# Kernel tuning notes

Hardware: AMD Instinct MI355X
Metric: run time of the kernel (lower is better)

## Reference

```python
import jax, jax.numpy as jnp
import numpy as np

N_NODES = 100000
N_EDGES = 3200000
N_GRAPHS = 1024
F_IN = 16
H = 64
N_CLASSES = 2
EPS = 1e-5


def _seg_sum(x, ids, n):
    return jax.ops.segment_sum(x, ids, num_segments=n, indices_are_sorted=True)


def graph_norm(x, batch, weight, bias, mean_scale, n_graphs):
    # PyG GraphNorm: per-graph mean (scaled by learnable mean_scale) and variance
    cnt = jnp.maximum(_seg_sum(jnp.ones((x.shape[0], 1), x.dtype), batch, n_graphs), 1.0)
    mean = _seg_sum(x, batch, n_graphs) / cnt                      # [G, F]
    out = x - mean[batch] * mean_scale                             # [N, F]
    var = _seg_sum(out * out, batch, n_graphs) / cnt               # [G, F]
    out = out / jnp.sqrt(var + EPS)[batch]
    return weight * out + bias


def graph_conv(x, src, dst, w_rel, b_rel, w_root):
    # PyG GraphConv (aggr='add'): lin_rel(sum_{j->i} x_j) + lin_root(x_i)
    agg = jax.ops.segment_sum(x[src], dst, num_segments=x.shape[0])  # [N, F_in]
    return agg @ w_rel.T + b_rel + x @ w_root.T


def setup_inputs():
    key = jax.random.key(0)
    ks = jax.random.split(key, 32)

    def lin(k, o, i):
        return jax.random.normal(k, (o, i), jnp.float32) * (1.0 / np.sqrt(i))

    inp = {}
    inp['x'] = jax.random.normal(ks[0], (N_NODES, F_IN), jnp.float32)
    inp['edge_index'] = jax.random.randint(ks[1], (2, N_EDGES), 0, N_NODES, jnp.int32)
    inp['batch'] = jnp.sort(jax.random.randint(ks[2], (N_NODES,), 0, N_GRAPHS, jnp.int32))
    # GraphNorm params (weight, bias, mean_scale), initialized as in PyG
    for name, f in (('gn0', F_IN), ('gn1', H), ('gn2', H)):
        inp[name + '_w'] = jnp.ones((f,), jnp.float32)
        inp[name + '_b'] = jnp.zeros((f,), jnp.float32)
        inp[name + '_ms'] = jnp.ones((f,), jnp.float32)
    # GraphConv params: lin_rel (with bias) + lin_root (no bias)
    inp['w1_rel'] = lin(ks[3], H, F_IN); inp['b1'] = jnp.zeros((H,), jnp.float32); inp['w1_root'] = lin(ks[4], H, F_IN)
    inp['w2_rel'] = lin(ks[5], H, H);    inp['b2'] = jnp.zeros((H,), jnp.float32); inp['w2_root'] = lin(ks[6], H, H)
    inp['w3_rel'] = lin(ks[7], H, H);    inp['b3'] = jnp.zeros((H,), jnp.float32); inp['w3_root'] = lin(ks[8], H, H)
    inp['dense_w'] = lin(ks[9], H, H); inp['dense_b'] = jnp.zeros((H,), jnp.float32)
    inp['out_w'] = lin(ks[10], N_CLASSES, H); inp['out_b'] = jnp.zeros((N_CLASSES,), jnp.float32)
    return inp


def reference(x, edge_index, batch,
              gn0_w, gn0_b, gn0_ms, gn1_w, gn1_b, gn1_ms, gn2_w, gn2_b, gn2_ms,
              w1_rel, b1, w1_root, w2_rel, b2, w2_root, w3_rel, b3, w3_root,
              dense_w, dense_b, out_w, out_b):
    src, dst = edge_index[0], edge_index[1]
    h = graph_norm(x, batch, gn0_w, gn0_b, gn0_ms, N_GRAPHS)
    h = jax.nn.relu(graph_conv(h, src, dst, w1_rel, b1, w1_root))
    h = graph_norm(h, batch, gn1_w, gn1_b, gn1_ms, N_GRAPHS)
    h = jax.nn.relu(graph_conv(h, src, dst, w2_rel, b2, w2_root))
    h = graph_norm(h, batch, gn2_w, gn2_b, gn2_ms, N_GRAPHS)
    h = jax.nn.relu(graph_conv(h, src, dst, w3_rel, b3, w3_root))
    # global_mean_pool
    cnt = jnp.maximum(_seg_sum(jnp.ones((h.shape[0], 1), h.dtype), batch, N_GRAPHS), 1.0)
    pooled = _seg_sum(h, batch, N_GRAPHS) / cnt                    # [G, 64]
    # dropout is identity in eval mode
    g = jax.nn.relu(pooled @ dense_w.T + dense_b)
    logits = g @ out_w.T + out_b
    return jax.nn.softmax(logits, axis=1)
```

## Files before the change

kernel.cpp:

```cpp
#include <hip/hip_runtime.h>

#define NG 1024
#define GN_EPS 1e-5f
#define BSHIFT 7

__device__ __forceinline__ float bf2f(unsigned short u) {
  union { float f; unsigned int i; } c;
  c.i = ((unsigned int)u) << 16;
  return c.f;
}
__device__ __forceinline__ unsigned short f2bf(float f) {
  union { float f; unsigned int i; } c;
  c.f = f;
  unsigned int b = c.i;
  b += 0x7fffu + ((b >> 16) & 1u);
  return (unsigned short)(b >> 16);
}
__device__ __forceinline__ void f4red(float4& a, int mask) {
  a.x += __shfl_xor(a.x, mask);
  a.y += __shfl_xor(a.y, mask);
  a.z += __shfl_xor(a.z, mask);
  a.w += __shfl_xor(a.w, mask);
}

__global__ void k_bounds(const int* __restrict__ batch, int* __restrict__ goff, int N) {
  int i = blockIdx.x * blockDim.x + threadIdx.x;
  if (i >= N) return;
  int b = batch[i];
  int pb = (i == 0) ? -1 : batch[i - 1];
  for (int g = pb + 1; g <= b; ++g) goff[g] = i;
  if (i == N - 1) {
    for (int g = b + 1; g <= NG; ++g) goff[g] = N;
  }
}

__global__ void k_hist(const int* __restrict__ dst, int* __restrict__ bucketCnt,
                       int E, int B) {
  __shared__ int h[1024];
  for (int i = threadIdx.x; i < B; i += 256) h[i] = 0;
  __syncthreads();
  for (int e = blockIdx.x * 256 + threadIdx.x; e < E; e += gridDim.x * 256)
    atomicAdd(&h[dst[e] >> BSHIFT], 1);
  __syncthreads();
  for (int i = threadIdx.x; i < B; i += 256)
    if (h[i]) atomicAdd(&bucketCnt[i], h[i]);
}

__global__ void k_bscan(const int* __restrict__ bucketCnt, int* __restrict__ bucketOff,
                        int* __restrict__ bucketCur, int B) {
  __shared__ int lds[1024];
  int t = threadIdx.x;
  int v = (t < B) ? bucketCnt[t] : 0;
  lds[t] = v;
  __syncthreads();
  for (int off = 1; off < 1024; off <<= 1) {
    int u = (t >= off) ? lds[t - off] : 0;
    __syncthreads();
    lds[t] += u;
    __syncthreads();
  }
  if (t < B) {
    int ex = lds[t] - v;
    bucketOff[t] = ex;
    bucketCur[t] = ex;
  }
}

__global__ __launch_bounds__(256) void k_binscatter(
    const int* __restrict__ src, const int* __restrict__ dst,
    int* __restrict__ bucketCur, unsigned int* __restrict__ ebuf,
    int E, int B, int C) {
  __shared__ int h[1024];
  __shared__ int cur[1024];
  int s = blockIdx.x * C;
  int e = min(s + C, E);
  if (s >= E) return;
  int t = threadIdx.x;
  for (int i = t; i < B; i += 256) h[i] = 0;
  __syncthreads();
  for (int k = s + t; k < e; k += 256) atomicAdd(&h[dst[k] >> BSHIFT], 1);
  __syncthreads();
  for (int i = t; i < B; i += 256) {
    int c = h[i];
    cur[i] = c ? atomicAdd(&bucketCur[i], c) : 0;
  }
  __syncthreads();
  for (int k = s + t; k < e; k += 256) {
    int d = dst[k];
    int b = d >> BSHIFT;
    int pos = atomicAdd(&cur[b], 1);
    ebuf[pos] = ((unsigned int)(d & 127) << 24) | (unsigned int)src[k];
  }
}

__global__ void k_bucket_fill(const unsigned int* __restrict__ ebuf,
                              const int* __restrict__ bucketOff,
                              int* __restrict__ rowptr, int* __restrict__ col,
                              int N, int E, int B) {
  __shared__ int deg[128];
  __shared__ int cur[128];
  int b = blockIdx.x;
  int s = bucketOff[b];
  int e = (b + 1 < B) ? bucketOff[b + 1] : E;
  int t = threadIdx.x;
  int base = b << BSHIFT;
  if (t < 128) deg[t] = 0;
  __syncthreads();
  for (int k = s + t; k < e; k += 256) atomicAdd(&deg[ebuf[k] >> 24], 1);
  __syncthreads();
  if (t == 0) {
    int acc = s;
    for (int i = 0; i < 128; ++i) {
      int d = deg[i];
      deg[i] = acc;
      acc += d;
    }
  }
  __syncthreads();
  if (t < 128) {
    cur[t] = deg[t];
    int idx = base + t;
    if (idx <= N) rowptr[idx] = deg[t];
  }
  __syncthreads();
  for (int k = s + t; k < e; k += 256) {
    unsigned int p = ebuf[k];
    int pos = atomicAdd(&cur[p >> 24], 1);
    col[pos] = (int)(p & 0x00ffffffu);
  }
}

template <int F>
__global__ void k_gn(const float* x, float* out, unsigned short* outbf,
                     const int* __restrict__ goff,
                     const float* __restrict__ w, const float* __restrict__ b,
                     const float* __restrict__ ms) {
  constexpr int NPW = 256 / F;
  __shared__ float r1[256], r2[256];
  __shared__ float sA[F], sB[F];
  int g = blockIdx.x;
  int s = goff[g], e = goff[g + 1];
  int t = threadIdx.x;
  int f = t % F, sub = t / F;
  float s1 = 0.f, s2 = 0.f;
  for (int i = s + sub; i < e; i += NPW) {
    float v = x[i * F + f];
    s1 += v;
    s2 += v * v;
  }
  r1[t] = s1;
  r2[t] = s2;
  __syncthreads();
  if (t < F) {
    float S1 = 0.f, S2 = 0.f;
    for (int k = 0; k < NPW; ++k) {
      S1 += r1[k * F + t];
      S2 += r2[k * F + t];
    }
    float cnt = (float)max(e - s, 1);
    float mean = S1 / cnt, m2 = S2 / cnt;
    float m = ms[t];
    float var = m2 + mean * mean * m * (m - 2.f);
    float rsq = rsqrtf(var + GN_EPS);
    float Av = w[t] * rsq;
    sA[t] = Av;
    sB[t] = b[t] - mean * m * Av;
  }
  __syncthreads();
  float Af = sA[f], Bf = sB[f];
  for (int i = s + sub; i < e; i += NPW) {
    float v = x[i * F + f] * Af + Bf;
    out[i * F + f] = v;
    outbf[i * F + f] = f2bf(v);
  }
}

template <int FIN>
__global__ __launch_bounds__(256) void k_conv(
    const float* __restrict__ hin, const unsigned short* __restrict__ hbf,
    float* __restrict__ hout,
    const int* __restrict__ rowptr, const int* __restrict__ col,
    const float* __restrict__ wrel, const float* __restrict__ brel,
    const float* __restrict__ wroot, int N) {
  constexpr int PAD = FIN + 4;
  constexpr int NSLOT = (FIN == 64) ? 4 : 16;
  __shared__ float aggL[64 * PAD];
  int tile = blockIdx.x;
  int lane = threadIdx.x & 63;
  int w = __builtin_amdgcn_readfirstlane(threadIdx.x >> 6);

  int q = (FIN == 64) ? (lane & 15) : (lane & 3);
  int slot = (FIN == 64) ? (lane >> 4) : (lane >> 2);

  for (int nl = 0; nl < 16; ++nl) {
    int r = w * 16 + nl;
    int n = tile * 64 + r;
    float4 a0 = make_float4(0.f, 0.f, 0.f, 0.f);
    float4 a1 = make_float4(0.f, 0.f, 0.f, 0.f);
    if (n < N) {
      int s = rowptr[n], e = rowptr[n + 1];
      int k = s + slot;
      for (; k + NSLOT < e; k += 2 * NSLOT) {
        int nb0 = col[k];
        int nb1 = col[k + NSLOT];
        ushort4 v0 = *(const ushort4*)&hbf[(size_t)nb0 * FIN + q * 4];
        ushort4 v1 = *(const ushort4*)&hbf[(size_t)nb1 * FIN + q * 4];
        a0.x += bf2f(v0.x); a0.y += bf2f(v0.y); a0.z += bf2f(v0.z); a0.w += bf2f(v0.w);
        a1.x += bf2f(v1.x); a1.y += bf2f(v1.y); a1.z += bf2f(v1.z); a1.w += bf2f(v1.w);
      }
      if (k < e) {
        int nb = col[k];
        ushort4 v = *(const ushort4*)&hbf[(size_t)nb * FIN + q * 4];
        a0.x += bf2f(v.x); a0.y += bf2f(v.y); a0.z += bf2f(v.z); a0.w += bf2f(v.w);
      }
    }
    a0.x += a1.x; a0.y += a1.y; a0.z += a1.z; a0.w += a1.w;
    if (FIN == 64) {
      f4red(a0, 16);
      f4red(a0, 32);
    } else {
      f4red(a0, 4);
      f4red(a0, 8);
      f4red(a0, 16);
      f4red(a0, 32);
    }
    if (slot == 0) *(float4*)&aggL[r * PAD + q * 4] = a0;
  }
  __syncthreads();

  int n = tile * 64 + lane;
  if (n >= N) return;
  int wbase = w * 16;
  float accR[16], accT[16];
#pragma unroll
  for (int j = 0; j < 16; ++j) {
    accR[j] = 0.f;
    accT[j] = 0.f;
  }
#pragma unroll 2
  for (int fq = 0; fq < FIN / 4; ++fq) {
    float4 qa = *(const float4*)&aggL[lane * PAD + fq * 4];
    float4 qh = *(const float4*)&hin[(size_t)n * FIN + fq * 4];
#pragma unroll
    for (int j = 0; j < 16; ++j) {
      int o = wbase + j;
      const float* wr = &wrel[o * FIN + fq * 4];
      const float* wt = &wroot[o * FIN + fq * 4];
      accR[j] += wr[0] * qa.x + wr[1] * qa.y + wr[2] * qa.z + wr[3] * qa.w;
      accT[j] += wt[0] * qh.x + wt[1] * qh.y + wt[2] * qh.z + wt[3] * qh.w;
    }
  }
#pragma unroll
  for (int qq = 0; qq < 4; ++qq) {
    float4 rv;
    float* rr = (float*)&rv;
#pragma unroll
    for (int jj = 0; jj < 4; ++jj) {
      int j = qq * 4 + jj;
      float v = accR[j] + accT[j] + brel[wbase + j];
      rr[jj] = fmaxf(v, 0.f);
    }
    *(float4*)&hout[(size_t)n * 64 + wbase + qq * 4] = rv;
  }
}

__global__ void k_final(const float* __restrict__ h, const int* __restrict__ goff,
                        const float* __restrict__ dw, const float* __restrict__ db,
                        const float* __restrict__ ow, const float* __restrict__ ob,
                        float* __restrict__ out) {
  __shared__ float red[256];
  __shared__ float pl[64];
  __shared__ float gl[64];
  int g = blockIdx.x;
  int s = goff[g], e = goff[g + 1];
  int t = threadIdx.x;
  int f = t & 63, sub = t >> 6;
  float s1 = 0.f;
  for (int i = s + sub; i < e; i += 4) s1 += h[i * 64 + f];
  red[t] = s1;
  __syncthreads();
  if (t < 64) {
    float S = red[t] + red[64 + t] + red[128 + t] + red[192 + t];
    float cnt = (float)max(e - s, 1);
    pl[t] = S / cnt;
  }
  __syncthreads();
  if (t < 64) {
    float acc = db[t];
#pragma unroll 8
    for (int k = 0; k < 64; ++k) acc += dw[t * 64 + k] * pl[k];
    gl[t] = fmaxf(acc, 0.f);
  }
  __syncthreads();
  if (t == 0) {
    float l0 = ob[0], l1 = ob[1];
    for (int k = 0; k < 64; ++k) {
      l0 += ow[k] * gl[k];
      l1 += ow[64 + k] * gl[k];
    }
    float m = fmaxf(l0, l1);
    float e0 = expf(l0 - m), e1 = expf(l1 - m);
    float inv = 1.f / (e0 + e1);
    out[g * 2 + 0] = e0 * inv;
    out[g * 2 + 1] = e1 * inv;
  }
}

extern "C" void kernel_launch(void* const* d_in, const int* in_sizes, int n_in,
                              void* d_out, int out_size, void* d_ws, size_t ws_size,
                              hipStream_t stream) {
  const float* x = (const float*)d_in[0];
  const int* ei = (const int*)d_in[1];
  const int* batch = (const int*)d_in[2];
  const float* gn0_w = (const float*)d_in[3];
  const float* gn0_b = (const float*)d_in[4];
  const float* gn0_ms = (const float*)d_in[5];
  const float* gn1_w = (const float*)d_in[6];
  const float* gn1_b = (const float*)d_in[7];
  const float* gn1_ms = (const float*)d_in[8];
  const float* gn2_w = (const float*)d_in[9];
  const float* gn2_b = (const float*)d_in[10];
  const float* gn2_ms = (const float*)d_in[11];
  const float* w1_rel = (const float*)d_in[12];
  const float* b1 = (const float*)d_in[13];
  const float* w1_root = (const float*)d_in[14];
  const float* w2_rel = (const float*)d_in[15];
  const float* b2 = (const float*)d_in[16];
  const float* w2_root = (const float*)d_in[17];
  const float* w3_rel = (const float*)d_in[18];
  const float* b3 = (const float*)d_in[19];
  const float* w3_root = (const float*)d_in[20];
  const float* dense_w = (const float*)d_in[21];
  const float* dense_b = (const float*)d_in[22];
  const float* out_w = (const float*)d_in[23];
  const float* out_b = (const float*)d_in[24];

  int N = in_sizes[2];
  int E = in_sizes[1] / 2;
  int B = (N >> BSHIFT) + 1;

  char* ws = (char*)d_ws;
  auto alloc = [&](size_t bytes) {
    char* p = ws;
    ws += (bytes + 255) & ~(size_t)255;
    return p;
  };
  int* rowptr = (int*)alloc(((size_t)N + 1) * 4);
  int* goff = (int*)alloc((NG + 1) * 4);
  int* bucketCnt = (int*)alloc((size_t)B * 4);
  int* bucketOff = (int*)alloc((size_t)B * 4);
  int* bucketCur = (int*)alloc((size_t)B * 4);
  int* col = (int*)alloc((size_t)E * 4);
  size_t hbytes = (size_t)N * 64 * 4;
  size_t ebytes = (size_t)E * 4;
  char* hA_raw = (char*)alloc(hbytes > ebytes ? hbytes : ebytes);
  float* hA = (float*)hA_raw;
  unsigned int* ebuf = (unsigned int*)hA_raw;
  float* hB = (float*)alloc(hbytes);
  unsigned short* hbf = (unsigned short*)alloc((size_t)N * 64 * 2);

  const int* src = ei;
  const int* dst = ei + E;

  hipMemsetAsync(bucketCnt, 0, (size_t)B * 4, stream);
  k_bounds<<<(N + 255) / 256, 256, 0, stream>>>(batch, goff, N);
  k_hist<<<256, 256, 0, stream>>>(dst, bucketCnt, E, B);
  k_bscan<<<1, 1024, 0, stream>>>(bucketCnt, bucketOff, bucketCur, B);
  int nbs = 192;
  int C = (E + nbs - 1) / nbs;
  k_binscatter<<<nbs, 256, 0, stream>>>(src, dst, bucketCur, ebuf, E, B, C);
  k_bucket_fill<<<B, 256, 0, stream>>>(ebuf, bucketOff, rowptr, col, N, E, B);

  int tiles = (N + 63) / 64;
  k_gn<16><<<NG, 256, 0, stream>>>(x, hA, hbf, goff, gn0_w, gn0_b, gn0_ms);
  k_conv<16><<<tiles, 256, 0, stream>>>(hA, hbf, hB, rowptr, col, w1_rel, b1, w1_root, N);
  k_gn<64><<<NG, 256, 0, stream>>>(hB, hB, hbf, goff, gn1_w, gn1_b, gn1_ms);
  k_conv<64><<<tiles, 256, 0, stream>>>(hB, hbf, hA, rowptr, col, w2_rel, b2, w2_root, N);
  k_gn<64><<<NG, 256, 0, stream>>>(hA, hA, hbf, goff, gn2_w, gn2_b, gn2_ms);
  k_conv<64><<<tiles, 256, 0, stream>>>(hA, hbf, hB, rowptr, col, w3_rel, b3, w3_root, N);
  k_final<<<NG, 256, 0, stream>>>(hB, goff, dense_w, dense_b, out_w, out_b, (float*)d_out);
}
```

Baseline: 573.2 us.

## Use 512-thread conv blocks with wider 16-byte bf16 gathers per lane

The GraphConv kernel now runs 8 waves per 64-node tile, each wave handling 8 nodes instead of 16, and each wave computes 8 output features instead of 16. For the 64-wide layers, each lane gathers 8 bf16 values (16 bytes) per neighbor across 8 edge slots, replacing 4 values across 4 slots. The aim is more memory-level parallelism in the irregular gather and more latency hiding. The cost is higher register and occupancy pressure from 512-thread blocks, plus an extra shuffle-reduction step for the 64-wide layers.

```diff
diff --git a/kernel.cpp b/kernel.cpp
--- a/kernel.cpp
+++ b/kernel.cpp
@@ -4,23 +4,34 @@
 #define GN_EPS 1e-5f
 #define BSHIFT 7
 
-__device__ __forceinline__ float bf2f(unsigned short u) {
-  union { float f; unsigned int i; } c;
-  c.i = ((unsigned int)u) << 16;
+typedef unsigned int u32;
+
+__device__ __forceinline__ float bflo(u32 u) {
+  union { float f; u32 i; } c;
+  c.i = u << 16;
   return c.f;
 }
+__device__ __forceinline__ float bfhi(u32 u) {
+  union { float f; u32 i; } c;
+  c.i = u & 0xffff0000u;
+  return c.f;
+}
 __device__ __forceinline__ unsigned short f2bf(float f) {
-  union { float f; unsigned int i; } c;
+  union { float f; u32 i; } c;
   c.f = f;
-  unsigned int b = c.i;
+  u32 b = c.i;
   b += 0x7fffu + ((b >> 16) & 1u);
   return (unsigned short)(b >> 16);
 }
-__device__ __forceinline__ void f4red(float4& a, int mask) {
-  a.x += __shfl_xor(a.x, mask);
-  a.y += __shfl_xor(a.y, mask);
-  a.z += __shfl_xor(a.z, mask);
-  a.w += __shfl_xor(a.w, mask);
+__device__ __forceinline__ void acc8(float* a, uint4 u) {
+  a[0] += bflo(u.x); a[1] += bfhi(u.x);
+  a[2] += bflo(u.y); a[3] += bfhi(u.y);
+  a[4] += bflo(u.z); a[5] += bfhi(u.z);
+  a[6] += bflo(u.w); a[7] += bfhi(u.w);
+}
+__device__ __forceinline__ void acc4(float* a, uint2 u) {
+  a[0] += bflo(u.x); a[1] += bfhi(u.x);
+  a[2] += bflo(u.y); a[3] += bfhi(u.y);
 }
 
 __global__ void k_bounds(const int* __restrict__ batch, int* __restrict__ goff, int N) {
@@ -68,7 +79,7 @@
 
 __global__ __launch_bounds__(256) void k_binscatter(
     const int* __restrict__ src, const int* __restrict__ dst,
-    int* __restrict__ bucketCur, unsigned int* __restrict__ ebuf,
+    int* __restrict__ bucketCur, u32* __restrict__ ebuf,
     int E, int B, int C) {
   __shared__ int h[1024];
   __shared__ int cur[1024];
@@ -89,11 +100,11 @@
     int d = dst[k];
     int b = d >> BSHIFT;
     int pos = atomicAdd(&cur[b], 1);
-    ebuf[pos] = ((unsigned int)(d & 127) << 24) | (unsigned int)src[k];
-  }
-}
-
-__global__ void k_bucket_fill(const unsigned int* __restrict__ ebuf,
+    ebuf[pos] = ((u32)(d & 127) << 24) | (u32)src[k];
+  }
+}
+
+__global__ void k_bucket_fill(const u32* __restrict__ ebuf,
                               const int* __restrict__ bucketOff,
                               int* __restrict__ rowptr, int* __restrict__ col,
                               int N, int E, int B) {
@@ -124,7 +135,7 @@
   }
   __syncthreads();
   for (int k = s + t; k < e; k += 256) {
-    unsigned int p = ebuf[k];
+    u32 p = ebuf[k];
     int pos = atomicAdd(&cur[p >> 24], 1);
     col[pos] = (int)(p & 0x00ffffffu);
   }
@@ -176,91 +187,104 @@
 }
 
 template <int FIN>
-__global__ __launch_bounds__(256) void k_conv(
-    const float* __restrict__ hin, const unsigned short* __restrict__ hbf,
+__global__ __launch_bounds__(512) void k_conv(
+    const float* __restrict__ hin, const u32* __restrict__ hbf,
     float* __restrict__ hout,
     const int* __restrict__ rowptr, const int* __restrict__ col,
     const float* __restrict__ wrel, const float* __restrict__ brel,
     const float* __restrict__ wroot, int N) {
   constexpr int PAD = FIN + 4;
-  constexpr int NSLOT = (FIN == 64) ? 4 : 16;
+  constexpr int CPR = FIN / 2;
+  constexpr int NSLOT = (FIN == 64) ? 8 : 16;
+  constexpr int NF = (FIN == 64) ? 8 : 4;
+  constexpr int FGL = 64 / NSLOT;
   __shared__ float aggL[64 * PAD];
   int tile = blockIdx.x;
   int lane = threadIdx.x & 63;
   int w = __builtin_amdgcn_readfirstlane(threadIdx.x >> 6);
 
-  int q = (FIN == 64) ? (lane & 15) : (lane & 3);
-  int slot = (FIN == 64) ? (lane >> 4) : (lane >> 2);
-
-  for (int nl = 0; nl < 16; ++nl) {
-    int r = w * 16 + nl;
+  int fg = (FIN == 64) ? (lane & 7) : (lane & 3);
+  int slot = (FIN == 64) ? (lane >> 3) : (lane >> 2);
+
+  for (int nl = 0; nl < 8; ++nl) {
+    int r = w * 8 + nl;
     int n = tile * 64 + r;
-    float4 a0 = make_float4(0.f, 0.f, 0.f, 0.f);
-    float4 a1 = make_float4(0.f, 0.f, 0.f, 0.f);
+    float a0[NF], a1[NF];
+#pragma unroll
+    for (int j = 0; j < NF; ++j) { a0[j] = 0.f; a1[j] = 0.f; }
     if (n < N) {
       int s = rowptr[n], e = rowptr[n + 1];
       int k = s + slot;
       for (; k + NSLOT < e; k += 2 * NSLOT) {
         int nb0 = col[k];
         int nb1 = col[k + NSLOT];
-        ushort4 v0 = *(const ushort4*)&hbf[(size_t)nb0 * FIN + q * 4];
-        ushort4 v1 = *(const ushort4*)&hbf[(size_t)nb1 * FIN + q * 4];
-        a0.x += bf2f(v0.x); a0.y += bf2f(v0.y); a0.z += bf2f(v0.z); a0.w += bf2f(v0.w);
-        a1.x += bf2f(v1.x); a1.y += bf2f(v1.y); a1.z += bf2f(v1.z); a1.w += bf2f(v1.w);
+        if (FIN == 64) {
+          uint4 u0 = *(const uint4*)&hbf[nb0 * CPR + fg * 4];
+          uint4 u1 = *(const uint4*)&hbf[nb1 * CPR + fg * 4];
+          acc8(a0, u0);
+          acc8(a1, u1);
+        } else {
+          uint2 u0 = *(const uint2*)&hbf[nb0 * CPR + fg * 2];
+          uint2 u1 = *(const uint2*)&hbf[nb1 * CPR + fg * 2];
+          acc4(a0, u0);
+          acc4(a1, u1);
+        }
       }
       if (k < e) {
         int nb = col[k];
-        ushort4 v = *(const ushort4*)&hbf[(size_t)nb * FIN + q * 4];
-        a0.x += bf2f(v.x); a0.y += bf2f(v.y); a0.z += bf2f(v.z); a0.w += bf2f(v.w);
+        if (FIN == 64) {
+          uint4 u = *(const uint4*)&hbf[nb * CPR + fg * 4];
+          acc8(a0, u);
+        } else {
+          uint2 u = *(const uint2*)&hbf[nb * CPR + fg * 2];
+          acc4(a0, u);
+        }
       }
     }
-    a0.x += a1.x; a0.y += a1.y; a0.z += a1.z; a0.w += a1.w;
-    if (FIN == 64) {
-      f4red(a0, 16);
-      f4red(a0, 32);
-    } else {
-      f4red(a0, 4);
-      f4red(a0, 8);
-      f4red(a0, 16);
-      f4red(a0, 32);
-    }
-    if (slot == 0) *(float4*)&aggL[r * PAD + q * 4] = a0;
+#pragma unroll
+    for (int j = 0; j < NF; ++j) a0[j] += a1[j];
+#pragma unroll
+    for (int m = FGL; m < 64; m <<= 1) {
+#pragma unroll
+      for (int j = 0; j < NF; ++j) a0[j] += __shfl_xor(a0[j], m);
+    }
+    if (slot == 0) {
+#pragma unroll
+      for (int j = 0; j < NF; j += 4)
+        *(float4*)&aggL[r * PAD + fg * NF + j] =
+            make_float4(a0[j], a0[j + 1], a0[j + 2], a0[j + 3]);
+    }
   }
   __syncthreads();
 
   int n = tile * 64 + lane;
   if (n >= N) return;
-  int wbase = w * 16;
-  float accR[16], accT[16];
-#pragma unroll
-  for (int j = 0; j < 16; ++j) {
-    accR[j] = 0.f;
-    accT[j] = 0.f;
-  }
-#pragma unroll 2
+  int j0 = w * 8;
+  float accR[8], accT[8];
+#pragma unroll
+  for (int j = 0; j < 8; ++j) { accR[j] = 0.f; accT[j] = 0.f; }
+#pragma unroll 4
   for (int fq = 0; fq < FIN / 4; ++fq) {
     float4 qa = *(const float4*)&aggL[lane * PAD + fq * 4];
     float4 qh = *(const float4*)&hin[(size_t)n * FIN + fq * 4];
 #pragma unroll
-    for (int j = 0; j < 16; ++j) {
-      int o = wbase + j;
-      const float* wr = &wrel[o * FIN + fq * 4];
-      const float* wt = &wroot[o * FIN + fq * 4];
+    for (int j = 0; j < 8; ++j) {
+      const float* wr = &wrel[(j0 + j) * FIN + fq * 4];
+      const float* wt = &wroot[(j0 + j) * FIN + fq * 4];
       accR[j] += wr[0] * qa.x + wr[1] * qa.y + wr[2] * qa.z + wr[3] * qa.w;
       accT[j] += wt[0] * qh.x + wt[1] * qh.y + wt[2] * qh.z + wt[3] * qh.w;
     }
   }
 #pragma unroll
-  for (int qq = 0; qq < 4; ++qq) {
+  for (int p = 0; p < 2; ++p) {
     float4 rv;
     float* rr = (float*)&rv;
 #pragma unroll
     for (int jj = 0; jj < 4; ++jj) {
-      int j = qq * 4 + jj;
-      float v = accR[j] + accT[j] + brel[wbase + j];
-      rr[jj] = fmaxf(v, 0.f);
-    }
-    *(float4*)&hout[(size_t)n * 64 + wbase + qq * 4] = rv;
+      int j = p * 4 + jj;
+      rr[jj] = fmaxf(accR[j] + accT[j] + brel[j0 + j], 0.f);
+    }
+    *(float4*)&hout[(size_t)n * 64 + j0 + p * 4] = rv;
   }
 }
 
@@ -355,7 +379,7 @@
   size_t ebytes = (size_t)E * 4;
   char* hA_raw = (char*)alloc(hbytes > ebytes ? hbytes : ebytes);
   float* hA = (float*)hA_raw;
-  unsigned int* ebuf = (unsigned int*)hA_raw;
+  u32* ebuf = (u32*)hA_raw;
   float* hB = (float*)alloc(hbytes);
   unsigned short* hbf = (unsigned short*)alloc((size_t)N * 64 * 2);
 
@@ -373,10 +397,10 @@
 
   int tiles = (N + 63) / 64;
   k_gn<16><<<NG, 256, 0, stream>>>(x, hA, hbf, goff, gn0_w, gn0_b, gn0_ms);
-  k_conv<16><<<tiles, 256, 0, stream>>>(hA, hbf, hB, rowptr, col, w1_rel, b1, w1_root, N);
+  k_conv<16><<<tiles, 512, 0, stream>>>(hA, (const u32*)hbf, hB, rowptr, col, w1_rel, b1, w1_root, N);
   k_gn<64><<<NG, 256, 0, stream>>>(hB, hB, hbf, goff, gn1_w, gn1_b, gn1_ms);
-  k_conv<64><<<tiles, 256, 0, stream>>>(hB, hbf, hA, rowptr, col, w2_rel, b2, w2_root, N);
+  k_conv<64><<<tiles, 512, 0, stream>>>(hB, (const u32*)hbf, hA, rowptr, col, w2_rel, b2, w2_root, N);
   k_gn<64><<<NG, 256, 0, stream>>>(hA, hA, hbf, goff, gn2_w, gn2_b, gn2_ms);
-  k_conv<64><<<tiles, 256, 0, stream>>>(hA, hbf, hB, rowptr, col, w3_rel, b3, w3_root, N);
+  k_conv<64><<<tiles, 512, 0, stream>>>(hA, (const u32*)hbf, hB, rowptr, col, w3_rel, b3, w3_root, N);
   k_final<<<NG, 256, 0, stream>>>(hB, goff, dense_w, dense_b, out_w, out_b, (float*)d_out);
 }
```

New measurement: 595.2 us. 3.8% more time.
